# Performance work log

Hardware: AMD Instinct MI355X
Metric: run time of the kernel (lower is better)

## Reference

```python
import jax, jax.numpy as jnp
import numpy as np

B, L, E, H = 32, 512, 1024, 1024


def setup_inputs() -> dict:
    key = jax.random.key(0)
    ks = jax.random.split(key, 12)
    s = 0.02
    return {
        "x": jax.random.normal(ks[0], (B, L, E), jnp.float32),
        "h0": jax.random.normal(ks[1], (B, L, H), jnp.float32),
        "c0": jax.random.normal(ks[2], (B, L, H), jnp.float32),
        "W_ioux": jax.random.normal(ks[3], (E, 3 * H), jnp.float32) * s,
        "W_iouh": jax.random.normal(ks[4], (2, H, 3 * H), jnp.float32) * s,
        "b_iouh": jax.random.normal(ks[5], (2, 3 * H), jnp.float32) * s,
        "W_fx": jax.random.normal(ks[6], (E, H), jnp.float32) * s,
        "W_fh": jax.random.normal(ks[7], (4, H, H), jnp.float32) * s,
        "b_fh": jax.random.normal(ks[8], (4, H), jnp.float32) * s,
        "tree_ids_d": jax.random.randint(ks[9], (B, L), 0, L, jnp.int32),
        "tree_ids_dr": jax.random.randint(ks[10], (B, L), 0, L, jnp.int32),
        "tree_ids_dl": jax.random.randint(ks[11], (B, L), 0, L, jnp.int32),
    }


def _scatter_add_rows(src, idx):
    # out[b, idx[b,l], :] += src[b, l, :]   (torch scatter_add_ on dim=1 with row-repeated index)
    b = jnp.arange(src.shape[0])[:, None]
    return jnp.zeros_like(src).at[b, idx].add(src)


def _gather_rows(src, idx):
    # out[b, l, :] = src[b, idx[b,l], :]    (torch gather on dim=1 with row-repeated index)
    return jnp.take_along_axis(src, idx[:, :, None], axis=1)


def _masked_scatter(dest, mask3, src):
    # torch masked_scatter_: True positions (flat order) filled with src elements in flat order
    mflat = mask3.reshape(-1)
    pos = jnp.cumsum(mflat.astype(jnp.int32)) - 1
    filled = jnp.take(src.reshape(-1), jnp.clip(pos, 0, src.size - 1))
    return jnp.where(mflat, filled, dest.reshape(-1)).reshape(dest.shape)


def reference(x, h0, c0, W_ioux, W_iouh, b_iouh, W_fx, W_fh, b_fh,
              tree_ids_d, tree_ids_dr, tree_ids_dl):
    Hh = h0.shape[-1]
    iou_x = x @ W_ioux                               # [B,L,3H]
    iou_hr = h0 @ W_iouh[0] + b_iouh[0]              # [B,L,3H]
    iou_hl = h0 @ W_iouh[1] + b_iouh[1]
    # original repeats index only to hidden_size -> only first H cols (i-gate) get scattered child states
    add = (_scatter_add_rows(iou_hr[..., :Hh], tree_ids_dr)
           + _scatter_add_rows(iou_hl[..., :Hh], tree_ids_dl))
    iou = iou_x.at[..., :Hh].add(add)
    i, o, u = jnp.split(iou, 3, axis=-1)
    i, o, u = jax.nn.sigmoid(i), jax.nn.sigmoid(o), jnp.tanh(u)

    fx = x @ W_fx                                    # [B,L,H]
    # fh[0],fh[1] both gathered at index_r; fh[2],fh[3] both at index_l -> fuse the GEMMs
    fr = h0 @ (W_fh[0] + W_fh[1]) + (b_fh[0] + b_fh[1])
    fl = h0 @ (W_fh[2] + W_fh[3]) + (b_fh[2] + b_fh[3])
    f = jax.nn.sigmoid(_gather_rows(fx, tree_ids_d)
                       + _gather_rows(fr, tree_ids_dr)
                       + _gather_rows(fl, tree_ids_dl))

    fc = f * c0
    c_new = i * u + _scatter_add_rows(fc, tree_ids_d)
    h_new = o * jnp.tanh(c_new)

    mask3 = jnp.broadcast_to((tree_ids_d != 0)[:, :, None], h_new.shape)
    h_out = _masked_scatter(h0, mask3, h_new)
    c_out = _masked_scatter(c0, mask3, c_new)
    return (h_out, c_out)
```

## Files before the change

### kernel.cpp

```cpp
#include <hip/hip_runtime.h>


#define ROWS 16384
#define HID  1024
#define KDIM 1024
#define NCOLS 4096
#define TM 128
#define TN 128
#define TK 32

typedef __attribute__((ext_vector_type(4))) int            i32x4;
typedef __attribute__((ext_vector_type(4))) float          f32x4;
typedef __attribute__((ext_vector_type(4))) unsigned short u16x4;

__device__ __forceinline__ unsigned short f2bf(float f) {
  unsigned u = __float_as_uint(f);
  unsigned r = 0x7FFFu + ((u >> 16) & 1u);
  return (unsigned short)((u + r) >> 16);
}
__device__ __forceinline__ float bf2f(unsigned short v) {
  return __uint_as_float(((unsigned)v) << 16);
}
__device__ __forceinline__ float sigmoidf_(float x) {
  return 1.0f / (1.0f + __expf(-x));
}
__device__ __forceinline__ void gload16(const void* g, void* l) {
  __builtin_amdgcn_global_load_lds(
      (const __attribute__((address_space(1))) void*)g,
      (__attribute__((address_space(3))) void*)l, 16, 0, 0);
}
__device__ __forceinline__ void mfma_bf16(f32x4& acc, i32x4 a, i32x4 b) {
  asm volatile("v_mfma_f32_16x16x32_bf16 %0, %1, %2, %0"
               : "+v"(acc) : "v"(a), "v"(b));
}


__global__ void pack_wx(const float* __restrict__ Wioux, const float* __restrict__ Wfx,
                        unsigned short* __restrict__ Wxt) {
  __shared__ float t[32][33];
  const int n0 = blockIdx.x * 32, k0 = blockIdx.y * 32;
  const int tx = threadIdx.x, ty = threadIdx.y;
  const int n = n0 + tx, k = k0 + ty;
  float v = (n < 3072) ? Wioux[(size_t)k * 3072 + n]
                       : Wfx[(size_t)k * 1024 + (n - 3072)];
  t[ty][tx] = v;
  __syncthreads();
  Wxt[(size_t)(n0 + ty) * KDIM + (k0 + tx)] = f2bf(t[tx][ty]);
}

__global__ void pack_wh(const float* __restrict__ Wiouh, const float* __restrict__ Wfh,
                        unsigned short* __restrict__ Wht) {
  __shared__ float t[32][33];
  const int n0 = blockIdx.x * 32, k0 = blockIdx.y * 32;
  const int tx = threadIdx.x, ty = threadIdx.y;
  const int n = n0 + tx, k = k0 + ty;
  float v;
  if (n < 1024)      v = Wiouh[(size_t)k * 3072 + n];
  else if (n < 2048) v = Wiouh[3145728u + (size_t)k * 3072 + (n - 1024)];
  else if (n < 3072) { const int c = n - 2048;
    v = Wfh[(size_t)k * 1024 + c] + Wfh[1048576u + (size_t)k * 1024 + c]; }
  else { const int c = n - 3072;
    v = Wfh[2097152u + (size_t)k * 1024 + c] + Wfh[3145728u + (size_t)k * 1024 + c]; }
  t[ty][tx] = v;
  __syncthreads();
  Wht[(size_t)(n0 + ty) * KDIM + (k0 + tx)] = f2bf(t[tx][ty]);
}

__global__ void pack_bias(const float* __restrict__ b_iouh, const float* __restrict__ b_fh,
                          float* __restrict__ bh) {
  const int n = blockIdx.x * 1024 + threadIdx.x;
  float v;
  if (n < 1024)      v = b_iouh[n];
  else if (n < 2048) v = b_iouh[3072 + (n - 1024)];
  else if (n < 3072) { const int c = n - 2048; v = b_fh[c] + b_fh[1024 + c]; }
  else { const int c = n - 3072; v = b_fh[2048 + c] + b_fh[3072 + c]; }
  bh[n] = v;
}

__global__ void convert_bf16(const float* __restrict__ x, const float* __restrict__ h0,
                             unsigned short* __restrict__ xb, unsigned short* __restrict__ hb) {
  const size_t i = ((size_t)blockIdx.x * 256 + threadIdx.x) * 4;
  const float4 a = *(const float4*)&x[i];
  const float4 b = *(const float4*)&h0[i];
  u16x4 av = { f2bf(a.x), f2bf(a.y), f2bf(a.z), f2bf(a.w) };
  u16x4 bv = { f2bf(b.x), f2bf(b.y), f2bf(b.z), f2bf(b.w) };
  *(u16x4*)&xb[i] = av;
  *(u16x4*)&hb[i] = bv;
}

__global__ __launch_bounds__(256)
void gemm_both(const unsigned short* __restrict__ xb, const unsigned short* __restrict__ hb,
               const unsigned short* __restrict__ Wxt, const unsigned short* __restrict__ Wht,
               unsigned short* __restrict__ gxb, unsigned short* __restrict__ ghb,
               const float* __restrict__ bhv) {
  __shared__ __align__(16) unsigned short As[TM * TK];
  __shared__ __align__(16) unsigned short Bs[TN * TK];

  const unsigned short* A;
  const unsigned short* Bt;
  unsigned short* Cp;
  const float* bias;
  if (blockIdx.z == 0) { A = xb; Bt = Wxt; Cp = gxb; bias = nullptr; }
  else                 { A = hb; Bt = Wht; Cp = ghb; bias = bhv; }

  const int tid = threadIdx.x;
  const int w = tid >> 6, lane = tid & 63;
  const int bm = blockIdx.y * TM, bn = blockIdx.x * TN;
  const int wm = (w & 1) * 64, wn = (w >> 1) * 64;
  const int m0 = lane & 15, kg = lane >> 4;

  const int srow = w * 16 + (lane >> 2);
  const int sseg = (lane & 3) * 8;
  const unsigned short* ga0 = A  + (size_t)(bm + srow) * KDIM + sseg;
  const unsigned short* ga1 = ga0 + (size_t)64 * KDIM;
  const unsigned short* gb0 = Bt + (size_t)(bn + srow) * KDIM + sseg;
  const unsigned short* gb1 = gb0 + (size_t)64 * KDIM;
  unsigned short* la0 = &As[(w * 16) * TK];
  unsigned short* la1 = &As[(64 + w * 16) * TK];
  unsigned short* lb0 = &Bs[(w * 16) * TK];
  unsigned short* lb1 = &Bs[(64 + w * 16) * TK];

  const int aoff = (wm + m0) * TK + kg * 8;
  const int boff = (wn + m0) * TK + kg * 8;

  f32x4 acc[4][4] = {};

  for (int k0 = 0; k0 < KDIM; k0 += TK) {
    gload16(ga0 + k0, la0);
    gload16(ga1 + k0, la1);
    gload16(gb0 + k0, lb0);
    gload16(gb1 + k0, lb1);
    __syncthreads();
    i32x4 af[4], bf[4];
#pragma unroll
    for (int i = 0; i < 4; ++i) af[i] = *(const i32x4*)&As[aoff + i * 16 * TK];
#pragma unroll
    for (int j = 0; j < 4; ++j) bf[j] = *(const i32x4*)&Bs[boff + j * 16 * TK];
#pragma unroll
    for (int i = 0; i < 4; ++i)
#pragma unroll
      for (int j = 0; j < 4; ++j)
        mfma_bf16(acc[i][j], af[i], bf[j]);
    __syncthreads();
  }

  const int rg = (lane >> 4) * 4;
#pragma unroll
  for (int i = 0; i < 4; ++i) {
#pragma unroll
    for (int j = 0; j < 4; ++j) {
      const int col = bn + wn + j * 16 + m0;
      const float bv = bias ? bias[col] : 0.0f;
      const int row = bm + wm + i * 16 + rg;
#pragma unroll
      for (int r = 0; r < 4; ++r)
        Cp[(size_t)(row + r) * NCOLS + col] = f2bf(acc[i][j][r] + bv);
    }
  }
}

__global__ void scan_mask(const int* __restrict__ idd, int* __restrict__ sel,
                          int* __restrict__ mcount) {
  __shared__ int ps[1024];
  const int t = threadIdx.x;
  int loc[16];
  int cnt = 0;
#pragma unroll
  for (int i = 0; i < 16; ++i) {
    const int v = (idd[t * 16 + i] != 0) ? 1 : 0;
    loc[i] = v; cnt += v;
  }
  ps[t] = cnt;
  __syncthreads();
  for (int off = 1; off < 1024; off <<= 1) {
    const int add = (t >= off) ? ps[t - off] : 0;
    __syncthreads();
    ps[t] += add;
    __syncthreads();
  }
  int rank = (t == 0) ? 0 : ps[t - 1];
#pragma unroll
  for (int i = 0; i < 16; ++i)
    if (loc[i]) sel[rank++] = t * 16 + i;
  if (t == 1023) *mcount = ps[1023];
}

__global__ void build_csr(const int* __restrict__ idd, const int* __restrict__ idr,
                          const int* __restrict__ idl,
                          int* __restrict__ ofsD, int* __restrict__ ofsR, int* __restrict__ ofsL,
                          int* __restrict__ lstD, int* __restrict__ lstR, int* __restrict__ lstL) {
  __shared__ int sidx[512];
  __shared__ int scan[512];
  const int b = blockIdx.x, t = threadIdx.x;
  const int gb = b << 9;
  const int* const srcs[3] = { idd, idr, idl };
  int* const ofss[3] = { ofsD, ofsR, ofsL };
  int* const lsts[3] = { lstD, lstR, lstL };
  for (int a = 0; a < 3; ++a) {
    sidx[t] = srcs[a][gb + t];
    scan[t] = 0;
    __syncthreads();
    atomicAdd(&scan[sidx[t]], 1);
    __syncthreads();
    int v = scan[t];
    for (int off = 1; off < 512; off <<= 1) {
      const int add = (t >= off) ? scan[t - off] : 0;
      __syncthreads();
      scan[t] += add;
      __syncthreads();
    }
    const int start = scan[t] - v;
    ofss[a][b * 513 + t] = start;
    if (t == 511) ofss[a][b * 513 + 512] = scan[511];
    int pos = start;
    for (int l = 0; l < 512; ++l)
      if (sidx[l] == t) lsts[a][gb + (pos++)] = l;
    __syncthreads();
  }
}

__global__ __launch_bounds__(256)
void fused_final(const unsigned short* __restrict__ gxb, const unsigned short* __restrict__ ghb,
                 const float* __restrict__ h0, const float* __restrict__ c0,
                 const int* __restrict__ idd, const int* __restrict__ idr,
                 const int* __restrict__ idl,
                 const int* __restrict__ ofsR, const int* __restrict__ lstR,
                 const int* __restrict__ ofsL, const int* __restrict__ lstL,
                 const int* __restrict__ ofsD, const int* __restrict__ lstD,
                 const int* __restrict__ sel, const int* __restrict__ mcount,
                 float* __restrict__ hout, float* __restrict__ cout, int r0) {
  const int r = blockIdx.x;
  const int g = r0 + r;
  const int j = g & 511;
  const int bb = g >> 9;
  const int lbase = (r >> 9) << 9;
  const int ob = bb * 513;
  const int lb = bb << 9;
  const int c = threadIdx.x << 2;

  float a0 = 0.f, a1 = 0.f, a2 = 0.f, a3 = 0.f;
  for (int q = ofsR[ob + j], e = ofsR[ob + j + 1]; q < e; ++q) {
    const int l = lstR[lb + q];
    const u16x4 v = *(const u16x4*)&ghb[(size_t)(lbase + l) * NCOLS + c];
    a0 += bf2f(v[0]); a1 += bf2f(v[1]); a2 += bf2f(v[2]); a3 += bf2f(v[3]);
  }
  for (int q = ofsL[ob + j], e = ofsL[ob + j + 1]; q < e; ++q) {
    const int l = lstL[lb + q];
    const u16x4 v = *(const u16x4*)&ghb[(size_t)(lbase + l) * NCOLS + 1024 + c];
    a0 += bf2f(v[0]); a1 += bf2f(v[1]); a2 += bf2f(v[2]); a3 += bf2f(v[3]);
  }

  const u16x4 fx4 = *(const u16x4*)&gxb[(size_t)r * NCOLS + 3072 + c];
  const float fx0 = bf2f(fx4[0]), fx1 = bf2f(fx4[1]), fx2 = bf2f(fx4[2]), fx3 = bf2f(fx4[3]);
  float fc0 = 0.f, fc1 = 0.f, fc2 = 0.f, fc3 = 0.f;
  for (int q = ofsD[ob + j], e = ofsD[ob + j + 1]; q < e; ++q) {
    const int l = lstD[lb + q];
    const int jr = idr[lb + l], jl = idl[lb + l];
    const u16x4 rv = *(const u16x4*)&ghb[(size_t)(lbase + jr) * NCOLS + 2048 + c];
    const u16x4 lv = *(const u16x4*)&ghb[(size_t)(lbase + jl) * NCOLS + 3072 + c];
    const float4 cc = *(const float4*)&c0[(size_t)(lb + l) * HID + c];
    fc0 += sigmoidf_(fx0 + bf2f(rv[0]) + bf2f(lv[0])) * cc.x;
    fc1 += sigmoidf_(fx1 + bf2f(rv[1]) + bf2f(lv[1])) * cc.y;
    fc2 += sigmoidf_(fx2 + bf2f(rv[2]) + bf2f(lv[2])) * cc.z;
    fc3 += sigmoidf_(fx3 + bf2f(rv[3]) + bf2f(lv[3])) * cc.w;
  }

  const u16x4 vi = *(const u16x4*)&gxb[(size_t)r * NCOLS + c];
  const u16x4 vo = *(const u16x4*)&gxb[(size_t)r * NCOLS + 1024 + c];
  const u16x4 vu = *(const u16x4*)&gxb[(size_t)r * NCOLS + 2048 + c];
  float4 hn, cn;
  {
    const float ig = sigmoidf_(bf2f(vi[0]) + a0), og = sigmoidf_(bf2f(vo[0]));
    cn.x = ig * tanhf(bf2f(vu[0])) + fc0; hn.x = og * tanhf(cn.x);
  }
  {
    const float ig = sigmoidf_(bf2f(vi[1]) + a1), og = sigmoidf_(bf2f(vo[1]));
    cn.y = ig * tanhf(bf2f(vu[1])) + fc1; hn.y = og * tanhf(cn.y);
  }
  {
    const float ig = sigmoidf_(bf2f(vi[2]) + a2), og = sigmoidf_(bf2f(vo[2]));
    cn.z = ig * tanhf(bf2f(vu[2])) + fc2; hn.z = og * tanhf(cn.z);
  }
  {
    const float ig = sigmoidf_(bf2f(vi[3]) + a3), og = sigmoidf_(bf2f(vo[3]));
    cn.w = ig * tanhf(bf2f(vu[3])) + fc3; hn.w = og * tanhf(cn.w);
  }

  if (idd[g] == 0) {
    *(float4*)&hout[(size_t)g * HID + c] = *(const float4*)&h0[(size_t)g * HID + c];
    *(float4*)&cout[(size_t)g * HID + c] = *(const float4*)&c0[(size_t)g * HID + c];
  }
  const int m = *mcount;
  if (g < m) {
    const int o = sel[g];
    *(float4*)&hout[(size_t)o * HID + c] = hn;
    *(float4*)&cout[(size_t)o * HID + c] = cn;
  }
}

extern "C" void kernel_launch(void* const* d_in, const int* in_sizes, int n_in,
                              void* d_out, int out_size, void* d_ws, size_t ws_size,
                              hipStream_t stream) {
  const float* x      = (const float*)d_in[0];
  const float* h0     = (const float*)d_in[1];
  const float* c0     = (const float*)d_in[2];
  const float* W_ioux = (const float*)d_in[3];
  const float* W_iouh = (const float*)d_in[4];
  const float* b_iouh = (const float*)d_in[5];
  const float* W_fx   = (const float*)d_in[6];
  const float* W_fh   = (const float*)d_in[7];
  const float* b_fh   = (const float*)d_in[8];
  const int* idd      = (const int*)d_in[9];
  const int* idr      = (const int*)d_in[10];
  const int* idl      = (const int*)d_in[11];
  float* hout = (float*)d_out;
  float* cout = hout + (size_t)ROWS * HID;

  char* ws = (char*)d_ws;
  unsigned short* Wxt  = (unsigned short*)(ws);
  unsigned short* Wht  = (unsigned short*)(ws + 8388608u);
  float*          bh   = (float*)(ws + 16777216u);
  int*            sel  = (int*)(ws + 16793600u);
  int*            mcnt = (int*)(ws + 16859136u);
  int*            ofsD = (int*)(ws + 16859392u);
  int*            ofsR = (int*)(ws + 16925184u);
  int*            ofsL = (int*)(ws + 16990976u);
  int*            lstD = (int*)(ws + 17056768u);
  int*            lstR = (int*)(ws + 17122304u);
  int*            lstL = (int*)(ws + 17187840u);
  const size_t    base = 17253376u;

  int C = 32;
  while (C > 1 && base + 10485760ull * (size_t)C > ws_size) C >>= 1;
  const int R = 512 * C;

  char* p = ws + base;
  unsigned short* xb  = (unsigned short*)p;  p += 1048576ull * C;
  unsigned short* hb  = (unsigned short*)p;  p += 1048576ull * C;
  unsigned short* gxb = (unsigned short*)p;  p += 4194304ull * C;
  unsigned short* ghb = (unsigned short*)p;

  pack_wx<<<dim3(128, 32), dim3(32, 32), 0, stream>>>(W_ioux, W_fx, Wxt);
  pack_wh<<<dim3(128, 32), dim3(32, 32), 0, stream>>>(W_iouh, W_fh, Wht);
  pack_bias<<<4, 1024, 0, stream>>>(b_iouh, b_fh, bh);
  scan_mask<<<1, 1024, 0, stream>>>(idd, sel, mcnt);
  build_csr<<<32, 512, 0, stream>>>(idd, idr, idl, ofsD, ofsR, ofsL, lstD, lstR, lstL);

  for (int b0 = 0; b0 < 32; b0 += C) {
    const size_t r0 = (size_t)b0 * 512;
    convert_bf16<<<R, 256, 0, stream>>>(x + r0 * HID, h0 + r0 * HID, xb, hb);
    gemm_both<<<dim3(NCOLS / TN, R / TM, 2), 256, 0, stream>>>(xb, hb, Wxt, Wht, gxb, ghb, bh);
    fused_final<<<R, 256, 0, stream>>>(gxb, ghb, h0, c0, idd, idr, idl,
                                       ofsR, lstR, ofsL, lstL, ofsD, lstD,
                                       sel, mcnt, hout, cout, (int)r0);
  }
}
```

Before: 561.7 us.

## Rewrite GEMM as 256x256x64 double-buffered 8-wave kernel with swizzled LDS

Replaces the 128x128x32 single-buffered bf16 MFMA GEMM with a 256x256 tile, BK=64 kernel using 8 waves, double-buffered LDS and XOR-swizzled rows to avoid bank conflicts. Global-to-LDS loads for the next K step are interleaved across four compute phases, with fine-grained vmcnt waits and s_setprio around the MFMA bursts. The goal is to hide memory latency and raise arithmetic intensity. In exchange it uses 128KB of LDS per block, which may limit occupancy, and relies on hand-counted waitcnt values being correct.

```diff
diff --git a/kernel.cpp b/kernel.cpp
--- a/kernel.cpp
+++ b/kernel.cpp
@@ -5,9 +5,9 @@
 #define HID  1024
 #define KDIM 1024
 #define NCOLS 4096
-#define TM 128
-#define TN 128
-#define TK 32
+#define BM 256
+#define BN 256
+#define BK 64
 
 typedef __attribute__((ext_vector_type(4))) int            i32x4;
 typedef __attribute__((ext_vector_type(4))) float          f32x4;
@@ -88,13 +88,55 @@
   *(u16x4*)&hb[i] = bv;
 }
 
-__global__ __launch_bounds__(256)
-void gemm_both(const unsigned short* __restrict__ xb, const unsigned short* __restrict__ hb,
-               const unsigned short* __restrict__ Wxt, const unsigned short* __restrict__ Wht,
-               unsigned short* __restrict__ gxb, unsigned short* __restrict__ ghb,
-               const float* __restrict__ bhv) {
-  __shared__ __align__(16) unsigned short As[TM * TK];
-  __shared__ __align__(16) unsigned short Bs[TN * TK];
+__device__ __forceinline__ void stage8(const unsigned short* __restrict__ gp,
+                                       unsigned short* __restrict__ lp,
+                                       int rowbase, int gbase, int k0, int lane) {
+  const int lrow = rowbase + (lane >> 3);
+  const int sseg = (lane & 7) ^ ((lane >> 3) & 7);
+  gload16(gp + (size_t)(gbase + lrow) * KDIM + k0 + sseg * 8,
+          lp + ((size_t)rowbase << 6));
+}
+
+#define PHASE(qm, qn, STAGES, VM)                                            \
+  {                                                                          \
+    i32x4 af[4][2], bfr[2][2];                                               \
+    const unsigned short* Ab = &S[b][0][0][0];                               \
+    const unsigned short* Bb = &S[b][1][0][0];                               \
+    _Pragma("unroll")                                                        \
+    for (int i = 0; i < 4; ++i) {                                            \
+      const int row = wr * 128 + (qm) * 64 + i * 16 + m0;                    \
+      _Pragma("unroll")                                                      \
+      for (int s = 0; s < 2; ++s)                                            \
+        af[i][s] = *(const i32x4*)(Ab + row * 64 + (((kg + s * 4) ^ sw8) << 3)); \
+    }                                                                        \
+    _Pragma("unroll")                                                        \
+    for (int j = 0; j < 2; ++j) {                                            \
+      const int col = wc * 64 + (qn) * 32 + j * 16 + m0;                     \
+      _Pragma("unroll")                                                      \
+      for (int s = 0; s < 2; ++s)                                            \
+        bfr[j][s] = *(const i32x4*)(Bb + col * 64 + (((kg + s * 4) ^ sw8) << 3)); \
+    }                                                                        \
+    STAGES;                                                                  \
+    VM;                                                                      \
+    __builtin_amdgcn_s_barrier();                                            \
+    __builtin_amdgcn_s_setprio(1);                                           \
+    _Pragma("unroll")                                                        \
+    for (int i = 0; i < 4; ++i)                                              \
+      _Pragma("unroll")                                                      \
+      for (int j = 0; j < 2; ++j) {                                          \
+        mfma_bf16(acc[(qm) * 4 + i][(qn) * 2 + j], af[i][0], bfr[j][0]);     \
+        mfma_bf16(acc[(qm) * 4 + i][(qn) * 2 + j], af[i][1], bfr[j][1]);     \
+      }                                                                      \
+    __builtin_amdgcn_s_setprio(0);                                           \
+    __builtin_amdgcn_s_barrier();                                            \
+  }
+
+__global__ __launch_bounds__(512, 2)
+void gemm8(const unsigned short* __restrict__ xb, const unsigned short* __restrict__ hb,
+           const unsigned short* __restrict__ Wxt, const unsigned short* __restrict__ Wht,
+           unsigned short* __restrict__ gxb, unsigned short* __restrict__ ghb,
+           const float* __restrict__ bhv) {
+  __shared__ __align__(16) unsigned short S[2][2][256][64];
 
   const unsigned short* A;
   const unsigned short* Bt;
@@ -103,58 +145,62 @@
   if (blockIdx.z == 0) { A = xb; Bt = Wxt; Cp = gxb; bias = nullptr; }
   else                 { A = hb; Bt = Wht; Cp = ghb; bias = bhv; }
 
-  const int tid = threadIdx.x;
-  const int w = tid >> 6, lane = tid & 63;
-  const int bm = blockIdx.y * TM, bn = blockIdx.x * TN;
-  const int wm = (w & 1) * 64, wn = (w >> 1) * 64;
-  const int m0 = lane & 15, kg = lane >> 4;
-
-  const int srow = w * 16 + (lane >> 2);
-  const int sseg = (lane & 3) * 8;
-  const unsigned short* ga0 = A  + (size_t)(bm + srow) * KDIM + sseg;
-  const unsigned short* ga1 = ga0 + (size_t)64 * KDIM;
-  const unsigned short* gb0 = Bt + (size_t)(bn + srow) * KDIM + sseg;
-  const unsigned short* gb1 = gb0 + (size_t)64 * KDIM;
-  unsigned short* la0 = &As[(w * 16) * TK];
-  unsigned short* la1 = &As[(64 + w * 16) * TK];
-  unsigned short* lb0 = &Bs[(w * 16) * TK];
-  unsigned short* lb1 = &Bs[(64 + w * 16) * TK];
-
-  const int aoff = (wm + m0) * TK + kg * 8;
-  const int boff = (wn + m0) * TK + kg * 8;
-
-  f32x4 acc[4][4] = {};
-
-  for (int k0 = 0; k0 < KDIM; k0 += TK) {
-    gload16(ga0 + k0, la0);
-    gload16(ga1 + k0, la1);
-    gload16(gb0 + k0, lb0);
-    gload16(gb1 + k0, lb1);
-    __syncthreads();
-    i32x4 af[4], bf[4];
+  const int tid = threadIdx.x, w = tid >> 6, lane = tid & 63;
+  const int wr = w >> 2, wc = w & 3;
+  const int bm = blockIdx.y * BM, bn = blockIdx.x * BN;
+  const int m0 = lane & 15, kg = lane >> 4, sw8 = m0 & 7;
+  const int bb0 = (w >> 2) * 64 + (w & 3) * 8;
+
+  f32x4 acc[8][4] = {};
+
+  stage8(A,  &S[0][0][0][0], w * 8,        bm, 0, lane);
+  stage8(A,  &S[0][0][0][0], 128 + w * 8,  bm, 0, lane);
+  stage8(A,  &S[0][0][0][0], 64 + w * 8,   bm, 0, lane);
+  stage8(A,  &S[0][0][0][0], 192 + w * 8,  bm, 0, lane);
+  stage8(Bt, &S[0][1][0][0], bb0,          bn, 0, lane);
+  stage8(Bt, &S[0][1][0][0], bb0 + 128,    bn, 0, lane);
+  stage8(Bt, &S[0][1][0][0], bb0 + 32,     bn, 0, lane);
+  stage8(Bt, &S[0][1][0][0], bb0 + 160,    bn, 0, lane);
+  asm volatile("s_waitcnt vmcnt(0)");
+  __builtin_amdgcn_s_barrier();
+
+  for (int t = 0; t < 16; ++t) {
+    const int b = t & 1, nb = b ^ 1;
+    const int k1 = (t + 1) << 6;
+    const bool st = (t < 15);
+    unsigned short* An = &S[nb][0][0][0];
+    unsigned short* Bn = &S[nb][1][0][0];
+
+    PHASE(0, 0,
+      { if (st) { stage8(A, An, w * 8, bm, k1, lane);
+                  stage8(A, An, 128 + w * 8, bm, k1, lane); } },
+      {});
+    PHASE(0, 1,
+      { if (st) { stage8(Bt, Bn, bb0, bn, k1, lane);
+                  stage8(Bt, Bn, bb0 + 128, bn, k1, lane); } },
+      { if (st) asm volatile("s_waitcnt vmcnt(4)");
+        else    asm volatile("s_waitcnt vmcnt(0)"); });
+    PHASE(1, 0,
+      { if (st) { stage8(Bt, Bn, bb0 + 32, bn, k1, lane);
+                  stage8(Bt, Bn, bb0 + 160, bn, k1, lane); } },
+      {});
+    PHASE(1, 1,
+      { if (st) { stage8(A, An, 64 + w * 8, bm, k1, lane);
+                  stage8(A, An, 192 + w * 8, bm, k1, lane); } },
+      { asm volatile("s_waitcnt vmcnt(2)"); });
+  }
+
+  const int rg = kg * 4;
 #pragma unroll
-    for (int i = 0; i < 4; ++i) af[i] = *(const i32x4*)&As[aoff + i * 16 * TK];
+  for (int mi = 0; mi < 8; ++mi) {
 #pragma unroll
-    for (int j = 0; j < 4; ++j) bf[j] = *(const i32x4*)&Bs[boff + j * 16 * TK];
-#pragma unroll
-    for (int i = 0; i < 4; ++i)
-#pragma unroll
-      for (int j = 0; j < 4; ++j)
-        mfma_bf16(acc[i][j], af[i], bf[j]);
-    __syncthreads();
-  }
-
-  const int rg = (lane >> 4) * 4;
-#pragma unroll
-  for (int i = 0; i < 4; ++i) {
-#pragma unroll
-    for (int j = 0; j < 4; ++j) {
-      const int col = bn + wn + j * 16 + m0;
+    for (int nj = 0; nj < 4; ++nj) {
+      const int col = bn + wc * 64 + nj * 16 + m0;
       const float bv = bias ? bias[col] : 0.0f;
-      const int row = bm + wm + i * 16 + rg;
+      const int row = bm + wr * 128 + mi * 16 + rg;
 #pragma unroll
       for (int r = 0; r < 4; ++r)
-        Cp[(size_t)(row + r) * NCOLS + col] = f2bf(acc[i][j][r] + bv);
+        Cp[(size_t)(row + r) * NCOLS + col] = f2bf(acc[mi][nj][r] + bv);
     }
   }
 }
@@ -349,7 +395,7 @@
   for (int b0 = 0; b0 < 32; b0 += C) {
     const size_t r0 = (size_t)b0 * 512;
     convert_bf16<<<R, 256, 0, stream>>>(x + r0 * HID, h0 + r0 * HID, xb, hb);
-    gemm_both<<<dim3(NCOLS / TN, R / TM, 2), 256, 0, stream>>>(xb, hb, Wxt, Wht, gxb, ghb, bh);
+    gemm8<<<dim3(NCOLS / BN, R / BM, 2), 512, 0, stream>>>(xb, hb, Wxt, Wht, gxb, ghb, bh);
     fused_final<<<R, 256, 0, stream>>>(gxb, ghb, h0, c0, idd, idr, idl,
                                        ofsR, lstR, ofsL, lstL, ofsD, lstD,
                                        sel, mcnt, hout, cout, (int)r0);
```

Result: no change. 552.8 us (-1.6%).

## Replace LDS-staged GEMM with direct global-to-register loads and XCD-aware block remap

Applied to the files above, without the earlier changes.

The GEMM no longer stages A/B tiles through shared memory with global_load_lds and two barriers per K step. Each wave instead loads its MFMA operand fragments straight from global memory into registers, with no synchronisation. A block-index remap groups row tiles per XCD so blocks sharing data land on the same L2, and launch bounds now request 3 blocks per CU. The cost is that data reuse across the four waves now relies on the L1/L2 caches instead of LDS, which may add redundant global traffic.

```diff
diff --git a/kernel.cpp b/kernel.cpp
--- a/kernel.cpp
+++ b/kernel.cpp
@@ -5,9 +5,6 @@
 #define HID  1024
 #define KDIM 1024
 #define NCOLS 4096
-#define TM 128
-#define TN 128
-#define TK 32
 
 typedef __attribute__((ext_vector_type(4))) int            i32x4;
 typedef __attribute__((ext_vector_type(4))) float          f32x4;
@@ -23,11 +20,6 @@
 }
 __device__ __forceinline__ float sigmoidf_(float x) {
   return 1.0f / (1.0f + __expf(-x));
-}
-__device__ __forceinline__ void gload16(const void* g, void* l) {
-  __builtin_amdgcn_global_load_lds(
-      (const __attribute__((address_space(1))) void*)g,
-      (__attribute__((address_space(3))) void*)l, 16, 0, 0);
 }
 __device__ __forceinline__ void mfma_bf16(f32x4& acc, i32x4 a, i32x4 b) {
   asm volatile("v_mfma_f32_16x16x32_bf16 %0, %1, %2, %0"
@@ -88,14 +80,11 @@
   *(u16x4*)&hb[i] = bv;
 }
 
-__global__ __launch_bounds__(256)
-void gemm_both(const unsigned short* __restrict__ xb, const unsigned short* __restrict__ hb,
-               const unsigned short* __restrict__ Wxt, const unsigned short* __restrict__ Wht,
-               unsigned short* __restrict__ gxb, unsigned short* __restrict__ ghb,
-               const float* __restrict__ bhv) {
-  __shared__ __align__(16) unsigned short As[TM * TK];
-  __shared__ __align__(16) unsigned short Bs[TN * TK];
-
+__global__ __launch_bounds__(256, 3)
+void gemm_nl(const unsigned short* __restrict__ xb, const unsigned short* __restrict__ hb,
+             const unsigned short* __restrict__ Wxt, const unsigned short* __restrict__ Wht,
+             unsigned short* __restrict__ gxb, unsigned short* __restrict__ ghb,
+             const float* __restrict__ bhv) {
   const unsigned short* A;
   const unsigned short* Bt;
   unsigned short* Cp;
@@ -103,55 +92,49 @@
   if (blockIdx.z == 0) { A = xb; Bt = Wxt; Cp = gxb; bias = nullptr; }
   else                 { A = hb; Bt = Wht; Cp = ghb; bias = bhv; }
 
-  const int tid = threadIdx.x;
-  const int w = tid >> 6, lane = tid & 63;
-  const int bm = blockIdx.y * TM, bn = blockIdx.x * TN;
-  const int wm = (w & 1) * 64, wn = (w >> 1) * 64;
+  int bx = blockIdx.x, by = blockIdx.y;
+  {
+    const int n = blockIdx.x + gridDim.x * blockIdx.y;
+    const int xcd = n & 7, idx = n >> 3;
+    const int ych = gridDim.y >> 3;
+    bx = idx / ych;
+    by = xcd * ych + (idx % ych);
+  }
+  const int tid = threadIdx.x, w = tid >> 6, lane = tid & 63;
+  const int wr = w & 1, wc = w >> 1;
   const int m0 = lane & 15, kg = lane >> 4;
-
-  const int srow = w * 16 + (lane >> 2);
-  const int sseg = (lane & 3) * 8;
-  const unsigned short* ga0 = A  + (size_t)(bm + srow) * KDIM + sseg;
-  const unsigned short* ga1 = ga0 + (size_t)64 * KDIM;
-  const unsigned short* gb0 = Bt + (size_t)(bn + srow) * KDIM + sseg;
-  const unsigned short* gb1 = gb0 + (size_t)64 * KDIM;
-  unsigned short* la0 = &As[(w * 16) * TK];
-  unsigned short* la1 = &As[(64 + w * 16) * TK];
-  unsigned short* lb0 = &Bs[(w * 16) * TK];
-  unsigned short* lb1 = &Bs[(64 + w * 16) * TK];
-
-  const int aoff = (wm + m0) * TK + kg * 8;
-  const int boff = (wn + m0) * TK + kg * 8;
+  const int bm = by * 128 + wr * 64;
+  const int bn = bx * 128 + wc * 64;
+
+  const unsigned short* Ap = A  + (size_t)(bm + m0) * KDIM + kg * 8;
+  const unsigned short* Bp = Bt + (size_t)(bn + m0) * KDIM + kg * 8;
 
   f32x4 acc[4][4] = {};
-
-  for (int k0 = 0; k0 < KDIM; k0 += TK) {
-    gload16(ga0 + k0, la0);
-    gload16(ga1 + k0, la1);
-    gload16(gb0 + k0, lb0);
-    gload16(gb1 + k0, lb1);
-    __syncthreads();
+#pragma unroll 2
+  for (int t = 0; t < 32; ++t) {
+    const int k0 = t * 32;
     i32x4 af[4], bf[4];
 #pragma unroll
-    for (int i = 0; i < 4; ++i) af[i] = *(const i32x4*)&As[aoff + i * 16 * TK];
-#pragma unroll
-    for (int j = 0; j < 4; ++j) bf[j] = *(const i32x4*)&Bs[boff + j * 16 * TK];
+    for (int i = 0; i < 4; ++i)
+      af[i] = *(const i32x4*)(Ap + (size_t)i * 16 * KDIM + k0);
+#pragma unroll
+    for (int j = 0; j < 4; ++j)
+      bf[j] = *(const i32x4*)(Bp + (size_t)j * 16 * KDIM + k0);
 #pragma unroll
     for (int i = 0; i < 4; ++i)
 #pragma unroll
       for (int j = 0; j < 4; ++j)
         mfma_bf16(acc[i][j], af[i], bf[j]);
-    __syncthreads();
-  }
-
-  const int rg = (lane >> 4) * 4;
+  }
+
+  const int rg = kg * 4;
 #pragma unroll
   for (int i = 0; i < 4; ++i) {
 #pragma unroll
     for (int j = 0; j < 4; ++j) {
-      const int col = bn + wn + j * 16 + m0;
+      const int col = bn + j * 16 + m0;
       const float bv = bias ? bias[col] : 0.0f;
-      const int row = bm + wm + i * 16 + rg;
+      const int row = bm + i * 16 + rg;
 #pragma unroll
       for (int r = 0; r < 4; ++r)
         Cp[(size_t)(row + r) * NCOLS + col] = f2bf(acc[i][j][r] + bv);
@@ -349,7 +332,7 @@
   for (int b0 = 0; b0 < 32; b0 += C) {
     const size_t r0 = (size_t)b0 * 512;
     convert_bf16<<<R, 256, 0, stream>>>(x + r0 * HID, h0 + r0 * HID, xb, hb);
-    gemm_both<<<dim3(NCOLS / TN, R / TM, 2), 256, 0, stream>>>(xb, hb, Wxt, Wht, gxb, ghb, bh);
+    gemm_nl<<<dim3(NCOLS / 128, R / 128, 2), 256, 0, stream>>>(xb, hb, Wxt, Wht, gxb, ghb, bh);
     fused_final<<<R, 256, 0, stream>>>(gxb, ghb, h0, c0, idd, idr, idl,
                                        ofsR, lstR, ofsL, lstL, ofsD, lstD,
                                        sel, mcnt, hout, cout, (int)r0);
```

After: 1.165 ms. 2.07x slower.
